# Kernel tuning notes

Hardware: AMD Instinct MI355X
Metric: run time of the kernel (lower is better)

The kernel has to match this reference:

```python
import jax, jax.numpy as jnp
import numpy as np

NUM_HEADS = 16
HEAD_DIM = 64
COMP_RATIO = 8


def setup_inputs() -> dict:
    key = jax.random.key(0)
    ks = jax.random.split(key, 6)
    d_model = NUM_HEADS * HEAD_DIM  # 1024
    B, S = 2, 8192
    scale = 1.0 / np.sqrt(d_model)
    x = jax.random.normal(ks[0], (B, S, d_model), dtype=jnp.float32)
    Wq = jax.random.normal(ks[1], (d_model, NUM_HEADS * HEAD_DIM), dtype=jnp.float32) * scale
    Wk = jax.random.normal(ks[2], (d_model, NUM_HEADS * HEAD_DIM), dtype=jnp.float32) * scale
    Wv = jax.random.normal(ks[3], (d_model, NUM_HEADS * HEAD_DIM), dtype=jnp.float32) * scale
    Wo = jax.random.normal(ks[4], (NUM_HEADS * HEAD_DIM, d_model), dtype=jnp.float32) * scale
    bq = jnp.zeros((NUM_HEADS * HEAD_DIM,), jnp.float32)
    bk = jnp.zeros((NUM_HEADS * HEAD_DIM,), jnp.float32)
    bv = jnp.zeros((NUM_HEADS * HEAD_DIM,), jnp.float32)
    bo = jnp.zeros((d_model,), jnp.float32)
    return {"x": x, "local_window_start": 4096, "Wq": Wq, "bq": bq,
            "Wk": Wk, "bk": bk, "Wv": Wv, "bv": bv, "Wo": Wo, "bo": bo}


def reference(x, local_window_start, Wq, bq, Wk, bk, Wv, bv, Wo, bo):
    B, S, D = x.shape
    H, Hd, R = NUM_HEADS, HEAD_DIM, COMP_RATIO
    if local_window_start <= R:
        return jnp.zeros_like(x)
    num_pools = local_window_start // R
    if num_pools == 0:
        return jnp.zeros_like(x)
    trunc = num_pools * R
    # avg-pool compression of tokens before the local window
    compressed = x[:, :trunc, :].reshape(B, num_pools, R, D).mean(axis=2)  # (B, P, D)
    # projections
    q = (x @ Wq + bq).reshape(B, S, H, Hd).transpose(0, 2, 1, 3)            # (B,H,S,Hd)
    k = (compressed @ Wk + bk).reshape(B, num_pools, H, Hd).transpose(0, 2, 1, 3)  # (B,H,P,Hd)
    v = (compressed @ Wv + bv).reshape(B, num_pools, H, Hd).transpose(0, 2, 1, 3)
    scale = 1.0 / jnp.sqrt(jnp.float32(Hd))
    scores = jnp.einsum('bhqd,bhkd->bhqk', q, k) * scale                    # (B,H,S,P)
    # causal mask: a query can attend to a pool only if the pool fully precedes it
    q_pos = jnp.arange(S)[:, None]
    pool_end = (jnp.arange(num_pools) + 1) * R
    mask = q_pos >= pool_end[None, :]                                       # (S, P)
    scores = jnp.where(mask[None, None], scores, -1e9)
    attn = jax.nn.softmax(scores, axis=-1)
    out = jnp.einsum('bhqk,bhkd->bhqd', attn, v)                            # (B,H,S,Hd)
    out = out.transpose(0, 2, 1, 3).reshape(B, S, H * Hd)
    return out @ Wo + bo
```

## Files before the change

### kernel.cpp

```cpp
#include <hip/hip_runtime.h>
#include <hip/hip_bf16.h>


typedef __attribute__((ext_vector_type(8))) short bf16x8;
typedef __attribute__((ext_vector_type(4))) short bf16x4;
typedef __attribute__((ext_vector_type(4))) float f32x4;

#define MFMA_BF16(a, b, c) __builtin_amdgcn_mfma_f32_16x16x32_bf16((a), (b), (c), 0, 0, 0)

__device__ __forceinline__ unsigned short f2bu(float x) {
  __hip_bfloat16 b = __float2bfloat16(x);
  return __builtin_bit_cast(unsigned short, b);
}

__device__ __forceinline__ float fexp2(float x) {
  float r;
  asm("v_exp_f32 %0, %1" : "=v"(r) : "v"(x));
  return r;
}

__device__ __forceinline__ void gload_lds16(const void* g, void* l) {
  __builtin_amdgcn_global_load_lds(
      (const __attribute__((address_space(1))) unsigned*)(g),
      (__attribute__((address_space(3))) unsigned*)(l), 16, 0, 0);
}

__device__ __forceinline__ unsigned ldsaddr(const void* p) {
  return (unsigned)(unsigned long long)(const __attribute__((address_space(3))) char*)p;
}

__global__ void cast_compress_kernel(const float* __restrict__ x,
                                     __hip_bfloat16* __restrict__ xb,
                                     __hip_bfloat16* __restrict__ cb) {
  const int blk = blockIdx.x;
  const int b = blk >> 10, g = blk & 1023;
  const int d = threadIdx.x * 4;
  const size_t rb = ((size_t)(b * 8192 + g * 8)) * 1024 + d;
  float4 a = {0.f, 0.f, 0.f, 0.f};
#pragma unroll
  for (int r = 0; r < 8; ++r) {
    const float4 v = *(const float4*)&x[rb + (size_t)r * 1024];
    ushort4 o;
    o.x = f2bu(v.x); o.y = f2bu(v.y); o.z = f2bu(v.z); o.w = f2bu(v.w);
    *(ushort4*)&xb[rb + (size_t)r * 1024] = o;
    a.x += v.x; a.y += v.y; a.z += v.z; a.w += v.w;
  }
  if (g < 512) {
    ushort4 o;
    o.x = f2bu(a.x * 0.125f); o.y = f2bu(a.y * 0.125f);
    o.z = f2bu(a.z * 0.125f); o.w = f2bu(a.w * 0.125f);
    *(ushort4*)&cb[((size_t)(b * 512 + g)) * 1024 + d] = o;
  }
}

__global__ void transpose_w_kernel(const float* __restrict__ w0, const float* __restrict__ w1,
                                   const float* __restrict__ w2, const float* __restrict__ w3,
                                   __hip_bfloat16* __restrict__ t0, __hip_bfloat16* __restrict__ t1,
                                   __hip_bfloat16* __restrict__ t2, __hip_bfloat16* __restrict__ t3) {
  const float* W; __hip_bfloat16* T;
  switch (blockIdx.z) {
    case 0: W = w0; T = t0; break;
    case 1: W = w1; T = t1; break;
    case 2: W = w2; T = t2; break;
    default: W = w3; T = t3; break;
  }
  __shared__ float tile[32][33];
  const int tx = threadIdx.x, ty = threadIdx.y;
  const int k0 = blockIdx.x * 32, n0 = blockIdx.y * 32;
#pragma unroll
  for (int j = 0; j < 4; ++j) {
    const int kk = ty + j * 8;
    tile[kk][tx] = W[(size_t)(k0 + kk) * 1024 + n0 + tx];
  }
  __syncthreads();
#pragma unroll
  for (int j = 0; j < 4; ++j) {
    const int nn = ty + j * 8;
    T[(size_t)(n0 + nn) * 1024 + k0 + tx] = __float2bfloat16(tile[tx][nn]);
  }
}


#define STAGE(SPTR, SROWBASE, STILE, SLDSOFF)                                  \
  {                                                                            \
    const int _t = (STILE) < NT ? (STILE) : 0;                                 \
    const size_t _kb = (size_t)_t * 128;                                       \
    gload_lds16((const char*)(SPTR) + ((size_t)((SROWBASE) + srow0) * K) * 2 + _kb + scb0, \
                ldsC + (SLDSOFF) + wave * 1024);                               \
    gload_lds16((const char*)(SPTR) + ((size_t)((SROWBASE) + srow0 + 64) * K) * 2 + _kb + scb0, \
                ldsC + (SLDSOFF) + 8192 + wave * 1024);                        \
  }

#define MM4(MR, AF0, AF1)                                                      \
  acc[MR][0] = MFMA_BF16(AF0, bf00, acc[MR][0]);                               \
  acc[MR][1] = MFMA_BF16(AF0, bf10, acc[MR][1]);                               \
  acc[MR][2] = MFMA_BF16(AF0, bf20, acc[MR][2]);                               \
  acc[MR][3] = MFMA_BF16(AF0, bf30, acc[MR][3]);                               \
  acc[MR][0] = MFMA_BF16(AF1, bf01, acc[MR][0]);                               \
  acc[MR][1] = MFMA_BF16(AF1, bf11, acc[MR][1]);                               \
  acc[MR][2] = MFMA_BF16(AF1, bf21, acc[MR][2]);                               \
  acc[MR][3] = MFMA_BF16(AF1, bf31, acc[MR][3]);

#define PHASE(QM, DB, LOADB, SPTR, SROWBASE, STILE, SLDSOFF, DOVM)             \
  {                                                                            \
    bf16x8 af0, af1, af2, af3;                                                 \
    const unsigned ab = Ab0 + (DB)*32768u + (QM)*4096u;                        \
    asm volatile("ds_read_b128 %0, %1" : "=v"(af0) : "v"(ab));                 \
    asm volatile("ds_read_b128 %0, %1" : "=v"(af1) : "v"(ab ^ 64u));           \
    asm volatile("ds_read_b128 %0, %1" : "=v"(af2) : "v"(ab + 2048u));         \
    asm volatile("ds_read_b128 %0, %1" : "=v"(af3) : "v"((ab + 2048u) ^ 64u)); \
    if (LOADB) {                                                               \
      const unsigned bb = Bb0 + (DB)*32768u;                                   \
      asm volatile("ds_read_b128 %0, %1" : "=v"(bf00) : "v"(bb));              \
      asm volatile("ds_read_b128 %0, %1" : "=v"(bf01) : "v"(bb ^ 64u));        \
      asm volatile("ds_read_b128 %0, %1" : "=v"(bf10) : "v"(bb + 2048u));      \
      asm volatile("ds_read_b128 %0, %1" : "=v"(bf11) : "v"((bb + 2048u) ^ 64u)); \
      asm volatile("ds_read_b128 %0, %1" : "=v"(bf20) : "v"(bb + 4096u));      \
      asm volatile("ds_read_b128 %0, %1" : "=v"(bf21) : "v"((bb + 4096u) ^ 64u)); \
      asm volatile("ds_read_b128 %0, %1" : "=v"(bf30) : "v"(bb + 6144u));      \
      asm volatile("ds_read_b128 %0, %1" : "=v"(bf31) : "v"((bb + 6144u) ^ 64u)); \
    }                                                                          \
    STAGE(SPTR, SROWBASE, STILE, SLDSOFF)                                      \
    asm volatile("s_barrier" ::: "memory");                                    \
    asm volatile("s_waitcnt lgkmcnt(0)" ::: "memory");                         \
    __builtin_amdgcn_sched_barrier(0);                                         \
    __builtin_amdgcn_s_setprio(1);                                             \
    MM4((QM)*2 + 0, af0, af1)                                                  \
    MM4((QM)*2 + 1, af2, af3)                                                  \
    __builtin_amdgcn_s_setprio(0);                                             \
    if (DOVM) asm volatile("s_waitcnt vmcnt(4)" ::: "memory");                 \
    asm volatile("s_barrier" ::: "memory");                                    \
  }

template <typename OUT_T>
__global__ __launch_bounds__(512, 2) void gemm256_kernel(
    const __hip_bfloat16* __restrict__ A, const __hip_bfloat16* __restrict__ Bt,
    const float* __restrict__ bias, OUT_T* __restrict__ C, int M, int N, int K) {
  __shared__ alignas(16) char lds[131072];
  char* ldsC = lds;
  const int tid = threadIdx.x;
  const int wave = tid >> 6, lane = tid & 63;
  const int l15 = lane & 15, lg = lane >> 4;
  const int wm = wave >> 2, wn = wave & 3;

  const int nwg = gridDim.x, cpx = nwg >> 3;
  const int bid = blockIdx.x;
  const int swz = (bid & 7) * cpx + (bid >> 3);
  const int ncol = N >> 8;
  const int bn = swz % ncol, bm = swz / ncol;
  const long brow = (long)bm * 256;
  const long bcol = (long)bn * 256;

  const int NT = K >> 6;
  const int NITER = K >> 7;

  const int o0 = wave * 1024 + lane * 16;
  const int srow0 = o0 >> 7;
  const int scb0 = (o0 & 127) ^ ((srow0 & 7) << 4);

  const unsigned LB = ldsaddr(lds);
  const int off0 = (lg * 16) ^ ((l15 & 7) << 4);
  const unsigned Ab0 = LB + wm * 16384u + l15 * 128u + off0;
  const unsigned Bb0 = LB + 65536u + (wn >> 1) * 16384u + (wn & 1) * 8192u + l15 * 128u + off0;

  f32x4 acc[8][4];
#pragma unroll
  for (int m = 0; m < 8; ++m)
#pragma unroll
    for (int n = 0; n < 4; ++n) acc[m][n] = (f32x4){0.f, 0.f, 0.f, 0.f};

  bf16x8 bf00, bf01, bf10, bf11, bf20, bf21, bf30, bf31;

  STAGE(Bt, bcol + 128, 0, 81920)
  STAGE(Bt, bcol,       0, 65536)
  STAGE(A,  brow,       0, 0)
  STAGE(A,  brow + 128, 0, 16384)
  STAGE(Bt, bcol + 128, 1, 114688)
  STAGE(Bt, bcol,       1, 98304)
  asm volatile("s_waitcnt vmcnt(4)" ::: "memory");
  asm volatile("s_barrier" ::: "memory");

  for (int i = 0; i < NITER; ++i) {
    const int t0 = 2 * i;
    PHASE(0, 0, true,  A,  brow,       t0 + 1, 32768,  false)
    PHASE(1, 0, false, A,  brow + 128, t0 + 1, 49152,  false)
    PHASE(2, 0, false, Bt, bcol + 128, t0 + 2, 81920,  false)
    PHASE(3, 0, false, Bt, bcol,       t0 + 2, 65536,  true)
    PHASE(0, 1, true,  A,  brow,       t0 + 2, 0,      false)
    PHASE(1, 1, false, A,  brow + 128, t0 + 2, 16384,  false)
    PHASE(2, 1, false, Bt, bcol + 128, t0 + 3, 114688, false)
    PHASE(3, 1, false, Bt, bcol,       t0 + 3, 98304,  true)
  }

#pragma unroll
  for (int nn = 0; nn < 4; ++nn) {
    const long col = bcol + wn * 64 + nn * 16 + l15;
    const float bv = bias[col];
#pragma unroll
    for (int mr = 0; mr < 8; ++mr) {
      const long row = brow + wm * 128 + mr * 16 + lg * 4;
#pragma unroll
      for (int j = 0; j < 4; ++j) {
        const float v = acc[mr][nn][j] + bv;
        if constexpr (sizeof(OUT_T) == 2)
          C[(row + j) * N + col] = __float2bfloat16(v);
        else
          C[(row + j) * N + col] = v;
      }
    }
  }
}

__global__ __launch_bounds__(256, 2) void gemm_bt_dual_kernel(
    const __hip_bfloat16* __restrict__ A,
    const __hip_bfloat16* __restrict__ Bt0, const float* __restrict__ b0,
    __hip_bfloat16* __restrict__ C0,
    const __hip_bfloat16* __restrict__ Bt1, const float* __restrict__ b1,
    __hip_bfloat16* __restrict__ C1, int M, int N, int K) {
  const int sel = blockIdx.x >= (unsigned)(N >> 7);
  const __hip_bfloat16* Bt = sel ? Bt1 : Bt0;
  const float* bias = sel ? b1 : b0;
  __hip_bfloat16* C = sel ? C1 : C0;
  const int bx = blockIdx.x - sel * (N >> 7);

  __shared__ alignas(16) __hip_bfloat16 As[128 * 32];
  __shared__ alignas(16) __hip_bfloat16 Bs[128 * 32];
  const int tid = threadIdx.x;
  const int wave = tid >> 6, lane = tid & 63;
  const int l15 = lane & 15, lg = lane >> 4;
  const long brow = (long)blockIdx.y * 128;
  const long bcol = (long)bx * 128;
  const int wr = (wave >> 1) * 64;
  const int wc = (wave & 1) * 64;

  f32x4 acc[4][4];
#pragma unroll
  for (int m = 0; m < 4; ++m)
#pragma unroll
    for (int n = 0; n < 4; ++n) acc[m][n] = (f32x4){0.f, 0.f, 0.f, 0.f};

  for (int kt = 0; kt < K; kt += 32) {
#pragma unroll
    for (int j = 0; j < 2; ++j) {
      const int seg = wave * 2 + j;
      const int o = seg * 1024;
      const int ob = o + lane * 16;
      const int row = ob >> 6;
      const int cb = ob & 63;
      gload_lds16((const char*)A + ((brow + row) * (long)K + kt) * 2 + cb, (char*)As + o);
      gload_lds16((const char*)Bt + ((bcol + row) * (long)K + kt) * 2 + cb, (char*)Bs + o);
    }
    __syncthreads();
    bf16x8 af[4], bfr[4];
#pragma unroll
    for (int m = 0; m < 4; ++m)
      af[m] = *(const bf16x8*)&As[(wr + m * 16 + l15) * 32 + lg * 8];
#pragma unroll
    for (int n = 0; n < 4; ++n)
      bfr[n] = *(const bf16x8*)&Bs[(wc + n * 16 + l15) * 32 + lg * 8];
#pragma unroll
    for (int m = 0; m < 4; ++m)
#pragma unroll
      for (int n = 0; n < 4; ++n)
        acc[m][n] = MFMA_BF16(af[m], bfr[n], acc[m][n]);
    __syncthreads();
  }

#pragma unroll
  for (int m = 0; m < 4; ++m)
#pragma unroll
    for (int n = 0; n < 4; ++n) {
      const long col = bcol + wc + n * 16 + l15;
      const float bv = bias[col];
#pragma unroll
      for (int r = 0; r < 4; ++r) {
        const long row = brow + wr + m * 16 + lg * 4 + r;
        C[row * N + col] = __float2bfloat16(acc[m][n][r] + bv);
      }
    }
}

__global__ __launch_bounds__(512, 2) void attn_kernel(
    const __hip_bfloat16* __restrict__ Q,
    const __hip_bfloat16* __restrict__ Km,
    const __hip_bfloat16* __restrict__ Vm,
    __hip_bfloat16* __restrict__ O) {
  __shared__ alignas(16) __hip_bfloat16 Ks[512 * 64];
  __shared__ alignas(16) __hip_bfloat16 VT[64 * 512];
  const int bh = blockIdx.x;
  const int b = bh >> 4, h = bh & 15;
  const int tid = threadIdx.x, wave = tid >> 6, lane = tid & 63;
  const int l15 = lane & 15, lg = lane >> 4;
  const char* Kbase = (const char*)(Km + (size_t)b * 512 * 1024 + h * 64);
  const char* Vbase = (const char*)(Vm + (size_t)b * 512 * 1024 + h * 64);
  char* KsB = (char*)Ks;
  char* VTB = (char*)VT;

#pragma unroll
  for (int j = 0; j < 8; ++j) {
    const int seg = wave * 8 + j;
    const int p = seg * 8 + (lane >> 3);
    const int cb = ((lane & 7) * 16) ^ ((p & 7) << 4);
    gload_lds16(Kbase + (size_t)p * 2048 + cb, KsB + seg * 1024);
  }
#pragma unroll
  for (int it = 0; it < 8; ++it) {
    const int c = tid + it * 512;
    const int p = c >> 3, d0 = (c & 7) * 8;
    uint4 vv = *(const uint4*)(Vbase + (size_t)p * 2048 + d0 * 2);
    const unsigned short* e = (const unsigned short*)&vv;
#pragma unroll
    for (int ei = 0; ei < 8; ++ei) {
      const int d = d0 + ei;
      *(unsigned short*)(VTB + d * 1024 + ((p * 2) ^ ((d & 7) << 4))) = e[ei];
    }
  }
  __syncthreads();

  constexpr float SC = 0.18033688011112042f;
  for (int itq = 0; itq < 4; ++itq) {
    const int q0 = (blockIdx.y + itq * 8) * 256 + wave * 32;
    const __hip_bfloat16* Qr0 = Q + ((size_t)(b * 8192 + q0 + l15)) * 1024 + h * 64;
    const __hip_bfloat16* Qr1 = Qr0 + (size_t)16 * 1024;
    const bf16x8 qa0 = *(const bf16x8*)(Qr0 + lg * 8);
    const bf16x8 qa1 = *(const bf16x8*)(Qr0 + 32 + lg * 8);
    const bf16x8 qb0 = *(const bf16x8*)(Qr1 + lg * 8);
    const bf16x8 qb1 = *(const bf16x8*)(Qr1 + 32 + lg * 8);

    float m0 = -3.0e38f, m1 = -3.0e38f, l0 = 0.f, l1 = 0.f;
    f32x4 o4[2][4];
#pragma unroll
    for (int g = 0; g < 2; ++g)
#pragma unroll
      for (int d = 0; d < 4; ++d) o4[g][d] = (f32x4){0.f, 0.f, 0.f, 0.f};

#pragma unroll
    for (int ch = 0; ch < 4; ++ch) {
      if (!(ch == 0 || q0 == 0 || q0 >= ch * 1024)) continue;

      f32x4 s[2][8];
#pragma unroll
      for (int cc = 0; cc < 8; ++cc) {
        const int p = ch * 128 + cc * 16 + l15;
        const int rb = p * 128;
        const int sw = (p & 7) << 4;
        const bf16x8 kf0 = *(const bf16x8*)(KsB + rb + ((lg * 16) ^ sw));
        const bf16x8 kf1 = *(const bf16x8*)(KsB + rb + ((lg * 16 + 64) ^ sw));
        f32x4 z0 = {0.f, 0.f, 0.f, 0.f};
        z0 = MFMA_BF16(kf0, qa0, z0);
        z0 = MFMA_BF16(kf1, qa1, z0);
        s[0][cc] = z0;
        f32x4 z1 = {0.f, 0.f, 0.f, 0.f};
        z1 = MFMA_BF16(kf0, qb0, z1);
        z1 = MFMA_BF16(kf1, qb1, z1);
        s[1][cc] = z1;
      }
      if (q0 < (ch + 1) * 1024) {
#pragma unroll
        for (int g = 0; g < 2; ++g) {
          const int qa = q0 + g * 16 + l15;
          const float mval = (qa >= 8) ? -3.0e38f : 0.f;
#pragma unroll
          for (int cc = 0; cc < 8; ++cc) {
            const int pb8 = (ch * 128 + cc * 16 + lg * 4 + 1) * 8;
#pragma unroll
            for (int r = 0; r < 4; ++r)
              if (qa < pb8 + r * 8) s[g][cc][r] = mval;
          }
        }
      }
      float c0 = -3.0e38f, c1 = -3.0e38f;
#pragma unroll
      for (int cc = 0; cc < 8; ++cc)
#pragma unroll
        for (int r = 0; r < 4; ++r) {
          c0 = fmaxf(c0, s[0][cc][r]);
          c1 = fmaxf(c1, s[1][cc][r]);
        }
      c0 = fmaxf(c0, __shfl_xor(c0, 16)); c0 = fmaxf(c0, __shfl_xor(c0, 32));
      c1 = fmaxf(c1, __shfl_xor(c1, 16)); c1 = fmaxf(c1, __shfl_xor(c1, 32));
      const float n0 = fmaxf(m0, c0), n1 = fmaxf(m1, c1);
      if (!__all((n0 == m0) & (n1 == m1))) {
        const float f0 = fexp2((m0 - n0) * SC);
        const float f1 = fexp2((m1 - n1) * SC);
        l0 *= f0; l1 *= f1;
#pragma unroll
        for (int d = 0; d < 4; ++d) { o4[0][d] *= f0; o4[1][d] *= f1; }
        m0 = n0; m1 = n1;
      }
      const float ms0 = m0 * SC, ms1 = m1 * SC;
#pragma unroll
      for (int cc = 0; cc < 8; ++cc)
#pragma unroll
        for (int r = 0; r < 4; ++r) {
          const float e0 = fexp2(fmaf(s[0][cc][r], SC, -ms0));
          const float e1 = fexp2(fmaf(s[1][cc][r], SC, -ms1));
          s[0][cc][r] = e0; l0 += e0;
          s[1][cc][r] = e1; l1 += e1;
        }
#pragma unroll
      for (int kc = 0; kc < 4; ++kc) {
        bf16x8 p0, p1;
#pragma unroll
        for (int r = 0; r < 4; ++r) {
          p0[r]     = (short)f2bu(s[0][kc * 2][r]);
          p0[4 + r] = (short)f2bu(s[0][kc * 2 + 1][r]);
          p1[r]     = (short)f2bu(s[1][kc * 2][r]);
          p1[4 + r] = (short)f2bu(s[1][kc * 2 + 1][r]);
        }
        const int pbase = ch * 128 + kc * 32;
#pragma unroll
        for (int db = 0; db < 4; ++db) {
          const int d = db * 16 + l15;
          const int rowb = d * 1024;
          const int sw = (d & 7) << 4;
          const bf16x4 v0 = *(const bf16x4*)(VTB + rowb + (((pbase + lg * 4) * 2) ^ sw));
          const bf16x4 v1 = *(const bf16x4*)(VTB + rowb + (((pbase + 16 + lg * 4) * 2) ^ sw));
          const bf16x8 af = {v0[0], v0[1], v0[2], v0[3], v1[0], v1[1], v1[2], v1[3]};
          o4[0][db] = MFMA_BF16(af, p0, o4[0][db]);
          o4[1][db] = MFMA_BF16(af, p1, o4[1][db]);
        }
      }
    }
#pragma unroll
    for (int g = 0; g < 2; ++g) {
      float t = g ? l1 : l0;
      t += __shfl_xor(t, 16);
      t += __shfl_xor(t, 32);
      const float inv = 1.f / t;
      __hip_bfloat16* Op =
          O + ((size_t)(b * 8192 + q0 + g * 16 + l15)) * 1024 + h * 64 + lg * 4;
#pragma unroll
      for (int db = 0; db < 4; ++db) {
        ushort4 w;
        w.x = f2bu(o4[g][db][0] * inv);
        w.y = f2bu(o4[g][db][1] * inv);
        w.z = f2bu(o4[g][db][2] * inv);
        w.w = f2bu(o4[g][db][3] * inv);
        *(ushort4*)(Op + db * 16) = w;
      }
    }
  }
}

extern "C" void kernel_launch(void* const* d_in, const int* in_sizes, int n_in,
                              void* d_out, int out_size, void* d_ws, size_t ws_size,
                              hipStream_t stream) {
  const float* x  = (const float*)d_in[0];
  const float* Wq = (const float*)d_in[2];
  const float* bq = (const float*)d_in[3];
  const float* Wk = (const float*)d_in[4];
  const float* bk = (const float*)d_in[5];
  const float* Wv = (const float*)d_in[6];
  const float* bv = (const float*)d_in[7];
  const float* Wo = (const float*)d_in[8];
  const float* bo = (const float*)d_in[9];
  float* out = (float*)d_out;

  constexpr size_t SZ_XB = (size_t)16384 * 1024 * 2;
  constexpr size_t SZ_WT = (size_t)1024 * 1024 * 2;
  constexpr size_t SZ_CB = (size_t)1024 * 1024 * 2;
  char* ws = (char*)d_ws;
  __hip_bfloat16* xb   = (__hip_bfloat16*)ws;
  __hip_bfloat16* WqT  = (__hip_bfloat16*)(ws + SZ_XB);
  __hip_bfloat16* WkT  = (__hip_bfloat16*)(ws + SZ_XB + SZ_WT);
  __hip_bfloat16* WvT  = (__hip_bfloat16*)(ws + SZ_XB + 2 * SZ_WT);
  __hip_bfloat16* WoT  = (__hip_bfloat16*)(ws + SZ_XB + 3 * SZ_WT);
  __hip_bfloat16* cbuf = (__hip_bfloat16*)(ws + SZ_XB + 4 * SZ_WT);
  __hip_bfloat16* Qb   = (__hip_bfloat16*)(ws + SZ_XB + 4 * SZ_WT + SZ_CB);
  __hip_bfloat16* Kb   = (__hip_bfloat16*)(ws + SZ_XB + 4 * SZ_WT + SZ_CB + SZ_XB);
  __hip_bfloat16* Vb   = (__hip_bfloat16*)(ws + SZ_XB + 4 * SZ_WT + SZ_CB + SZ_XB + SZ_CB);

  cast_compress_kernel<<<dim3(2048), dim3(256), 0, stream>>>(x, xb, cbuf);
  transpose_w_kernel<<<dim3(32, 32, 4), dim3(32, 8), 0, stream>>>(
      Wq, Wk, Wv, Wo, WqT, WkT, WvT, WoT);
  gemm256_kernel<__hip_bfloat16><<<dim3(256), dim3(512), 0, stream>>>(
      xb, WqT, bq, Qb, 16384, 1024, 1024);
  gemm_bt_dual_kernel<<<dim3(16, 8), dim3(256), 0, stream>>>(
      cbuf, WkT, bk, Kb, WvT, bv, Vb, 1024, 1024, 1024);
  attn_kernel<<<dim3(32, 8), dim3(512), 0, stream>>>(Qb, Kb, Vb, xb);
  gemm256_kernel<float><<<dim3(256), dim3(512), 0, stream>>>(
      xb, WoT, bo, out, 16384, 1024, 1024);
}
```

Before: 178.9 us.

## Write V transposed from projection GEMM and read it directly in attention

The K/V projection kernel now stores V in a per-(batch, head) transposed layout, so the attention kernel no longer stages and transposes V into shared memory and reads PV operands straight from global memory. This halves LDS use per block, which may raise occupancy. The attention grid doubles along y and each block processes two query tiles paired from opposite ends of the sequence, balancing causal work. The cost is uncached global reads in the PV inner loop, which rely on L1/L2 hits.

```diff
diff --git a/kernel.cpp b/kernel.cpp
--- a/kernel.cpp
+++ b/kernel.cpp
@@ -216,11 +216,10 @@
     const __hip_bfloat16* __restrict__ Bt0, const float* __restrict__ b0,
     __hip_bfloat16* __restrict__ C0,
     const __hip_bfloat16* __restrict__ Bt1, const float* __restrict__ b1,
-    __hip_bfloat16* __restrict__ C1, int M, int N, int K) {
+    __hip_bfloat16* __restrict__ Vt, int M, int N, int K) {
   const int sel = blockIdx.x >= (unsigned)(N >> 7);
   const __hip_bfloat16* Bt = sel ? Bt1 : Bt0;
   const float* bias = sel ? b1 : b0;
-  __hip_bfloat16* C = sel ? C1 : C0;
   const int bx = blockIdx.x - sel * (N >> 7);
 
   __shared__ alignas(16) __hip_bfloat16 As[128 * 32];
@@ -272,10 +271,20 @@
     for (int n = 0; n < 4; ++n) {
       const long col = bcol + wc + n * 16 + l15;
       const float bv = bias[col];
-#pragma unroll
-      for (int r = 0; r < 4; ++r) {
-        const long row = brow + wr + m * 16 + lg * 4 + r;
-        C[row * N + col] = __float2bfloat16(acc[m][n][r] + bv);
+      const long row0 = brow + wr + m * 16 + lg * 4;
+      if (!sel) {
+#pragma unroll
+        for (int r = 0; r < 4; ++r)
+          C0[(row0 + r) * N + col] = __float2bfloat16(acc[m][n][r] + bv);
+      } else {
+        const int bb = (int)(row0 >> 9);
+        const int p = (int)(row0 & 511);
+        ushort4 w;
+        w.x = f2bu(acc[m][n][0] + bv);
+        w.y = f2bu(acc[m][n][1] + bv);
+        w.z = f2bu(acc[m][n][2] + bv);
+        w.w = f2bu(acc[m][n][3] + bv);
+        *(ushort4*)&Vt[((size_t)(bb * 1024 + col)) * 512 + p] = w;
       }
     }
 }
@@ -283,18 +292,21 @@
 __global__ __launch_bounds__(512, 2) void attn_kernel(
     const __hip_bfloat16* __restrict__ Q,
     const __hip_bfloat16* __restrict__ Km,
-    const __hip_bfloat16* __restrict__ Vm,
+    const __hip_bfloat16* __restrict__ Vt,
     __hip_bfloat16* __restrict__ O) {
   __shared__ alignas(16) __hip_bfloat16 Ks[512 * 64];
-  __shared__ alignas(16) __hip_bfloat16 VT[64 * 512];
   const int bh = blockIdx.x;
   const int b = bh >> 4, h = bh & 15;
   const int tid = threadIdx.x, wave = tid >> 6, lane = tid & 63;
   const int l15 = lane & 15, lg = lane >> 4;
   const char* Kbase = (const char*)(Km + (size_t)b * 512 * 1024 + h * 64);
-  const char* Vbase = (const char*)(Vm + (size_t)b * 512 * 1024 + h * 64);
   char* KsB = (char*)Ks;
-  char* VTB = (char*)VT;
+
+  const char* VtP = (const char*)(Vt + (size_t)bh * 32768);
+  const char* Vp0 = VtP + (size_t)(0 * 16 + l15) * 1024 + lg * 8;
+  const char* Vp1 = VtP + (size_t)(1 * 16 + l15) * 1024 + lg * 8;
+  const char* Vp2 = VtP + (size_t)(2 * 16 + l15) * 1024 + lg * 8;
+  const char* Vp3 = VtP + (size_t)(3 * 16 + l15) * 1024 + lg * 8;
 
 #pragma unroll
   for (int j = 0; j < 8; ++j) {
@@ -303,23 +315,21 @@
     const int cb = ((lane & 7) * 16) ^ ((p & 7) << 4);
     gload_lds16(Kbase + (size_t)p * 2048 + cb, KsB + seg * 1024);
   }
-#pragma unroll
-  for (int it = 0; it < 8; ++it) {
-    const int c = tid + it * 512;
-    const int p = c >> 3, d0 = (c & 7) * 8;
-    uint4 vv = *(const uint4*)(Vbase + (size_t)p * 2048 + d0 * 2);
-    const unsigned short* e = (const unsigned short*)&vv;
-#pragma unroll
-    for (int ei = 0; ei < 8; ++ei) {
-      const int d = d0 + ei;
-      *(unsigned short*)(VTB + d * 1024 + ((p * 2) ^ ((d & 7) << 4))) = e[ei];
-    }
-  }
   __syncthreads();
 
+#define PVDB(VPTR, DB)                                                         \
+  {                                                                            \
+    const bf16x4 v0 = *(const bf16x4*)((VPTR) + voff);                         \
+    const bf16x4 v1 = *(const bf16x4*)((VPTR) + voff + 32);                    \
+    const bf16x8 af = {v0[0], v0[1], v0[2], v0[3], v1[0], v1[1], v1[2], v1[3]};\
+    o4[0][DB] = MFMA_BF16(af, p0, o4[0][DB]);                                  \
+    o4[1][DB] = MFMA_BF16(af, p1, o4[1][DB]);                                  \
+  }
+
   constexpr float SC = 0.18033688011112042f;
-  for (int itq = 0; itq < 4; ++itq) {
-    const int q0 = (blockIdx.y + itq * 8) * 256 + wave * 32;
+  for (int itq = 0; itq < 2; ++itq) {
+    const int sidx = itq == 0 ? blockIdx.y : 31 - blockIdx.y;
+    const int q0 = sidx * 256 + wave * 32;
     const __hip_bfloat16* Qr0 = Q + ((size_t)(b * 8192 + q0 + l15)) * 1024 + h * 64;
     const __hip_bfloat16* Qr1 = Qr0 + (size_t)16 * 1024;
     const bf16x8 qa0 = *(const bf16x8*)(Qr0 + lg * 8);
@@ -408,18 +418,11 @@
           p1[r]     = (short)f2bu(s[1][kc * 2][r]);
           p1[4 + r] = (short)f2bu(s[1][kc * 2 + 1][r]);
         }
-        const int pbase = ch * 128 + kc * 32;
-#pragma unroll
-        for (int db = 0; db < 4; ++db) {
-          const int d = db * 16 + l15;
-          const int rowb = d * 1024;
-          const int sw = (d & 7) << 4;
-          const bf16x4 v0 = *(const bf16x4*)(VTB + rowb + (((pbase + lg * 4) * 2) ^ sw));
-          const bf16x4 v1 = *(const bf16x4*)(VTB + rowb + (((pbase + 16 + lg * 4) * 2) ^ sw));
-          const bf16x8 af = {v0[0], v0[1], v0[2], v0[3], v1[0], v1[1], v1[2], v1[3]};
-          o4[0][db] = MFMA_BF16(af, p0, o4[0][db]);
-          o4[1][db] = MFMA_BF16(af, p1, o4[1][db]);
-        }
+        const int voff = ch * 256 + kc * 64;
+        PVDB(Vp0, 0)
+        PVDB(Vp1, 1)
+        PVDB(Vp2, 2)
+        PVDB(Vp3, 3)
       }
     }
 #pragma unroll
@@ -441,6 +444,7 @@
       }
     }
   }
+#undef PVDB
 }
 
 extern "C" void kernel_launch(void* const* d_in, const int* in_sizes, int n_in,
@@ -469,7 +473,7 @@
   __hip_bfloat16* cbuf = (__hip_bfloat16*)(ws + SZ_XB + 4 * SZ_WT);
   __hip_bfloat16* Qb   = (__hip_bfloat16*)(ws + SZ_XB + 4 * SZ_WT + SZ_CB);
   __hip_bfloat16* Kb   = (__hip_bfloat16*)(ws + SZ_XB + 4 * SZ_WT + SZ_CB + SZ_XB);
-  __hip_bfloat16* Vb   = (__hip_bfloat16*)(ws + SZ_XB + 4 * SZ_WT + SZ_CB + SZ_XB + SZ_CB);
+  __hip_bfloat16* Vtb  = (__hip_bfloat16*)(ws + SZ_XB + 4 * SZ_WT + SZ_CB + SZ_XB + SZ_CB);
 
   cast_compress_kernel<<<dim3(2048), dim3(256), 0, stream>>>(x, xb, cbuf);
   transpose_w_kernel<<<dim3(32, 32, 4), dim3(32, 8), 0, stream>>>(
@@ -477,8 +481,8 @@
   gemm256_kernel<__hip_bfloat16><<<dim3(256), dim3(512), 0, stream>>>(
       xb, WqT, bq, Qb, 16384, 1024, 1024);
   gemm_bt_dual_kernel<<<dim3(16, 8), dim3(256), 0, stream>>>(
-      cbuf, WkT, bk, Kb, WvT, bv, Vb, 1024, 1024, 1024);
-  attn_kernel<<<dim3(32, 8), dim3(512), 0, stream>>>(Qb, Kb, Vb, xb);
+      cbuf, WkT, bk, Kb, WvT, bv, Vtb, 1024, 1024, 1024);
+  attn_kernel<<<dim3(32, 16), dim3(512), 0, stream>>>(Qb, Kb, Vtb, xb);
   gemm256_kernel<float><<<dim3(256), dim3(512), 0, stream>>>(
       xb, WoT, bo, out, 16384, 1024, 1024);
 }
```

New measurement: 240.5 us. 34.4% more time.
